# Kernel tuning notes

Hardware: AMD Instinct MI355X
Metric: run time of the kernel (lower is better)

Reference implementation:

```python
import jax, jax.numpy as jnp
import numpy as np

DIM = 256
HEADS = 4
WIN = 128
PAD = (WIN - 1) // 2  # 63
SHIFT = WIN // 2      # 64
RED = 16              # SE reduction


def _hann(w):
    # torch.hann_window(w, periodic=False)
    n = jnp.arange(w, dtype=jnp.float32)
    return 0.5 * (1.0 - jnp.cos(2.0 * jnp.pi * n / (w - 1)))


def _layernorm(x, g, b, eps=1e-5):
    mu = jnp.mean(x, axis=-1, keepdims=True)
    var = jnp.var(x, axis=-1, keepdims=True)
    return (x - mu) * jax.lax.rsqrt(var + eps) * g + b


def _attend_windows(x, ln_g, ln_b, in_proj_w, in_proj_b, out_w, out_b):
    B, T, C = x.shape
    w = WIN
    h = HEADS
    d = C // h
    L = T + 2 * PAD - w + 1  # number of stride-1 windows (= T-1 for even w)
    y = _layernorm(x, ln_g, ln_b)
    y_pad = jnp.pad(y, ((0, 0), (PAD, PAD), (0, 0)))
    idx = jnp.arange(L)[:, None] + jnp.arange(w)[None, :]  # (L, w)
    win = y_pad[:, idx, :]  # (B, L, w, C) -- the unfold blowup
    win = win * _hann(w)[None, None, :, None]
    # fused qkv projection (torch MHA in_proj)
    qkv = jnp.einsum('blwc,ec->blwe', win, in_proj_w) + in_proj_b  # (B,L,w,3C)
    q, k, v = jnp.split(qkv, 3, axis=-1)
    q = q.reshape(B, L, w, h, d)
    k = k.reshape(B, L, w, h, d)
    v = v.reshape(B, L, w, h, d)
    scale = 1.0 / jnp.sqrt(jnp.asarray(d, dtype=x.dtype))
    scores = jnp.einsum('blqhd,blkhd->blhqk', q, k) * scale
    attn = jax.nn.softmax(scores, axis=-1)
    o = jnp.einsum('blhqk,blkhd->blqhd', attn, v).reshape(B, L, w, C)
    o = jnp.einsum('blwc,ec->blwe', o, out_w) + out_b  # out_proj
    # fold: overlap-add back to length T (crop padding)
    idx_flat = idx.reshape(-1)  # (L*w,)
    acc = jnp.zeros((B, T + 2 * PAD, C), dtype=x.dtype)
    acc = acc.at[:, idx_flat, :].add(o.reshape(B, L * w, C))
    y_out = acc[:, PAD:PAD + T, :]
    counts = jnp.zeros((T + 2 * PAD,), dtype=x.dtype).at[idx_flat].add(1.0)
    counts = counts[PAD:PAD + T]
    return y_out / (counts[None, :, None] + 1e-6)


def setup_inputs() -> dict:
    key = jax.random.key(0)
    ks = jax.random.split(key, 9)
    C = DIM
    s = 0.02
    return {
        'x': jax.random.normal(ks[0], (1, 1024, C), dtype=jnp.float32),
        'ln_g': jnp.ones((C,), jnp.float32),
        'ln_b': jnp.zeros((C,), jnp.float32),
        'in_proj_w': jax.random.normal(ks[1], (3 * C, C), jnp.float32) * s,
        'in_proj_b': jnp.zeros((3 * C,), jnp.float32),
        'out_w': jax.random.normal(ks[2], (C, C), jnp.float32) * s,
        'out_b': jnp.zeros((C,), jnp.float32),
        'proj_w': jax.random.normal(ks[3], (C, C), jnp.float32) * s,
        'proj_b': jnp.zeros((C,), jnp.float32),
        'se_w1': jax.random.normal(ks[4], (C // RED, C), jnp.float32) * s,
        'se_w2': jax.random.normal(ks[5], (C, C // RED), jnp.float32) * s,
    }


def reference(x, ln_g, ln_b, in_proj_w, in_proj_b, out_w, out_b, proj_w, proj_b, se_w1, se_w2):
    # T > window_size branch (1024 > 128)
    y_main = _attend_windows(x, ln_g, ln_b, in_proj_w, in_proj_b, out_w, out_b)
    x_shift = jnp.roll(x, SHIFT, axis=1)
    y_shift = _attend_windows(x_shift, ln_g, ln_b, in_proj_w, in_proj_b, out_w, out_b)
    y_shift = jnp.roll(y_shift, -SHIFT, axis=1)
    y = 0.5 * (y_main + y_shift)
    y = jnp.einsum('btc,ec->bte', y, proj_w) + proj_b  # proj (dropout p=0 -> identity)
    # SE module: global average over T, bottleneck MLP, sigmoid gate
    s = jnp.mean(y, axis=1)  # (B, C)
    s = jax.nn.relu(s @ se_w1.T)
    s = jax.nn.sigmoid(s @ se_w2.T)
    y = y * s[:, None, :]
    return x + y
```

## Files before the change

### kernel.cpp

```cpp
#include <hip/hip_runtime.h>

#define TLEN 1024
#define CDIM 256
#define NHEAD 4
#define HD 64
#define WIN_ 128
#define PADL 63
#define LWIN 1023
#define TPAD 1150
#define SW 32

typedef __attribute__((ext_vector_type(8))) short bf16x8;
typedef __attribute__((ext_vector_type(4))) float f32x4;

__device__ __forceinline__ int prow(int v, int t) {
  if (v == 0) return t;
  if (t < PADL || t >= PADL + TLEN) return t;
  int s = t - PADL;
  s = (s + (TLEN - 64)) & (TLEN - 1);
  return PADL + s;
}

__device__ __forceinline__ float hannf(int j) {
  return 0.5f * (1.0f - __cosf(6.283185307179586f * (float)j / 127.0f));
}

__device__ __forceinline__ float countf(int t) {
  int lo = t - 127; if (lo < 0) lo = 0;
  int hi = t;       if (hi > LWIN - 1) hi = LWIN - 1;
  return (float)(hi - lo + 1);
}

__device__ __forceinline__ unsigned short bfr(float f) {
  unsigned int u = __float_as_uint(f);
  u += 0x7FFFu + ((u >> 16) & 1u);
  return (unsigned short)(u >> 16);
}
__device__ __forceinline__ unsigned int pk2t(float a, float b) {
  return __builtin_amdgcn_perm(__float_as_uint(b), __float_as_uint(a), 0x07060302u);
}
__device__ __forceinline__ float bfu(unsigned short u) {
  return __uint_as_float(((unsigned int)u) << 16);
}
__device__ __forceinline__ float bflo(unsigned int u) { return __uint_as_float(u << 16); }
__device__ __forceinline__ float bfhi(unsigned int u) { return __uint_as_float(u & 0xFFFF0000u); }

__device__ __forceinline__ float ex2(float x) {
  float r;
  asm("v_exp_f32 %0, %1" : "=v"(r) : "v"(x));
  return r;
}

#define AL16(h, l) ((((unsigned int)(l)) >> 16) | (((unsigned int)(h)) << 16))

#define QLOG2E 0.18033688011112042f

__global__ void k_prep(const float* __restrict__ x, const float* __restrict__ g,
                       const float* __restrict__ b, unsigned short* __restrict__ lnbf,
                       const float* __restrict__ W, unsigned short* __restrict__ Wb,
                       const float* __restrict__ pw, const float* __restrict__ ow,
                       const float* __restrict__ ob, unsigned short* __restrict__ Mtb,
                       float* __restrict__ vbv,
                       float* __restrict__ accg, unsigned short* __restrict__ Pbf,
                       float* __restrict__ msum) {
  __shared__ float pr[256];
  __shared__ float red[256];
  const int bid = blockIdx.x;
  const int tid = threadIdx.x;
  if (bid < 256) {
    int wv = tid >> 6, lane = tid & 63;
    int r = bid * 4 + wv;
    float4 v = ((const float4*)(x + (size_t)r * CDIM))[lane];
    float s = v.x + v.y + v.z + v.w;
    float q = v.x * v.x + v.y * v.y + v.z * v.z + v.w * v.w;
    #pragma unroll
    for (int m = 32; m >= 1; m >>= 1) { s += __shfl_xor(s, m); q += __shfl_xor(q, m); }
    float mu = s * (1.0f / 256.0f);
    float var = q * (1.0f / 256.0f) - mu * mu;
    float rs = rsqrtf(var + 1e-5f);
    float4 gg = ((const float4*)g)[lane];
    float4 bb = ((const float4*)b)[lane];
    uint2 o;
    o.x = (unsigned int)bfr((v.x - mu) * rs * gg.x + bb.x) |
          ((unsigned int)bfr((v.y - mu) * rs * gg.y + bb.y) << 16);
    o.y = (unsigned int)bfr((v.z - mu) * rs * gg.z + bb.z) |
          ((unsigned int)bfr((v.w - mu) * rs * gg.w + bb.w) << 16);
    ((uint2*)(lnbf + (size_t)r * CDIM))[lane] = o;
  } else if (bid < 352) {
    int i = (bid - 256) * 256 + tid;
    const float4* src = (const float4*)W;
    float4 a = src[2 * i], c = src[2 * i + 1];
    uint4 o;
    o.x = (unsigned int)bfr(a.x) | ((unsigned int)bfr(a.y) << 16);
    o.y = (unsigned int)bfr(a.z) | ((unsigned int)bfr(a.w) << 16);
    o.z = (unsigned int)bfr(c.x) | ((unsigned int)bfr(c.y) << 16);
    o.w = (unsigned int)bfr(c.z) | ((unsigned int)bfr(c.w) << 16);
    ((uint4*)Wb)[i] = o;
  } else if (bid < 608) {
    const int e = bid - 352;
    pr[tid] = pw[(size_t)e * CDIM + tid];
    __syncthreads();
    float a0 = 0.f, a1 = 0.f, a2 = 0.f, a3 = 0.f;
    for (int m = 0; m < 256; m += 4) {
      a0 += pr[m] * ow[(size_t)m * CDIM + tid];
      a1 += pr[m + 1] * ow[(size_t)(m + 1) * CDIM + tid];
      a2 += pr[m + 2] * ow[(size_t)(m + 2) * CDIM + tid];
      a3 += pr[m + 3] * ow[(size_t)(m + 3) * CDIM + tid];
    }
    Mtb[(size_t)e * CDIM + tid] = bfr((a0 + a1) + (a2 + a3));
    red[tid] = pr[tid] * ob[tid];
    __syncthreads();
    for (int s = 128; s > 0; s >>= 1) { if (tid < s) red[tid] += red[tid + s]; __syncthreads(); }
    if (tid == 0) vbv[e] = red[0];
  } else if (bid < 624) {
    uint4 zz = make_uint4(0, 0, 0, 0);
    for (int i = (bid - 608) * 256 + tid; i < 147200; i += 16 * 256)
      ((uint4*)accg)[i] = zz;
  } else {
    uint4 zz = make_uint4(0, 0, 0, 0);
    for (int i = (bid - 624) * 256 + tid; i < 12096; i += 16 * 256) {
      int idx = (i < 6048) ? i : (104352 + (i - 6048));
      ((uint4*)Pbf)[idx] = zz;
    }
    if (bid == 624 && tid < 64) ((float4*)msum)[tid] = make_float4(0.f, 0.f, 0.f, 0.f);
  }
}

__launch_bounds__(512, 1)
__global__ void k_proj(const unsigned short* __restrict__ lnbf,
                       const unsigned short* __restrict__ Wb,
                       unsigned short* __restrict__ Pbf) {
  __shared__ __align__(16) unsigned short Ps[64 * 128];
  const int tid = threadIdx.x;
  const int lane = tid & 63, wv = tid >> 6;
  const int li16 = lane & 15, q4 = lane >> 4;
  const int ws = wv & 1, we = wv >> 1;
  const int sbase = blockIdx.x * 64;
  const int ebase = blockIdx.y * 128;
  const int s0 = sbase + ws * 32;
  const int e0 = ebase + we * 32;

  f32x4 acc[2][2];
  #pragma unroll
  for (int it = 0; it < 2; ++it)
    #pragma unroll
    for (int et = 0; et < 2; ++et) acc[it][et] = (f32x4){0.f, 0.f, 0.f, 0.f};

  #pragma unroll
  for (int ks = 0; ks < 8; ++ks) {
    bf16x8 Af[2], Bf[2];
    #pragma unroll
    for (int it = 0; it < 2; ++it)
      Af[it] = *(const bf16x8*)(lnbf + (size_t)(s0 + 16 * it + li16) * 256 + ks * 32 + q4 * 8);
    #pragma unroll
    for (int et = 0; et < 2; ++et)
      Bf[et] = *(const bf16x8*)(Wb + (size_t)(e0 + 16 * et + li16) * 256 + ks * 32 + q4 * 8);
    #pragma unroll
    for (int it = 0; it < 2; ++it)
      #pragma unroll
      for (int et = 0; et < 2; ++et)
        acc[it][et] = __builtin_amdgcn_mfma_f32_16x16x32_bf16(Af[it], Bf[et], acc[it][et], 0, 0, 0);
  }
  #pragma unroll
  for (int it = 0; it < 2; ++it)
    #pragma unroll
    for (int et = 0; et < 2; ++et)
      #pragma unroll
      for (int r = 0; r < 4; ++r) {
        int lr = ws * 32 + 16 * it + 4 * q4 + r;
        int lc = we * 32 + 16 * et + li16;
        Ps[lr * 128 + lc] = bfr(acc[it][et][r]);
      }
  __syncthreads();
  for (int i = tid; i < 1024; i += 512) {
    int r = i >> 4, c = (i & 15) * 8;
    *(uint4*)(Pbf + (size_t)(PADL + sbase + r) * 768 + ebase + c) = *(uint4*)&Ps[r * 128 + c];
  }
}

__device__ __forceinline__ void stage_load(const unsigned short* __restrict__ Pbf,
                                           int v, int hd, int l0, int w, int tid,
                                           uint4& A, uint4& B) {
  const int jp = tid & 63;
  const int dg = tid >> 6;
  const int j0 = 2 * jp;
  int row0 = prow(v, l0 + w + j0);
  int row1 = prow(v, l0 + w + j0 + 1);
  A = *(const uint4*)(Pbf + (size_t)row0 * 768 + 512 + hd * 64 + dg * 8);
  B = *(const uint4*)(Pbf + (size_t)row1 * 768 + 512 + hd * 64 + dg * 8);
}

__device__ __forceinline__ void stage_write(unsigned short* vt, int w, int tid,
                                            const float* __restrict__ bB,
                                            const float* __restrict__ hth,
                                            uint4 a, uint4 b) {
  const int jp = tid & 63;
  const int dg = tid >> 6;
  const int j0 = 2 * jp;
  const int p0 = w + j0;
  float h0 = hth[j0], h1 = hth[j0 + 1];
  float e0 = ex2(h0 * bB[p0]);
  float e1 = ex2(h1 * bB[p0 + 1]);
  float f0 = e0 * h0, f1 = e1 * h1;
  unsigned int av[4] = {a.x, a.y, a.z, a.w};
  unsigned int bv[4] = {b.x, b.y, b.z, b.w};
  #pragma unroll
  for (int q = 0; q < 4; ++q) {
    int d0 = dg * 8 + 2 * q;
    unsigned int w0 = pk2t(f0 * bflo(av[q]), f1 * bflo(bv[q]));
    unsigned int w1 = pk2t(f0 * bfhi(av[q]), f1 * bfhi(bv[q]));
    *(unsigned int*)&vt[d0 * 128 + (j0 ^ ((d0 & 7) << 3))] = w0;
    *(unsigned int*)&vt[(d0 + 1) * 128 + (j0 ^ (((d0 + 1) & 7) << 3))] = w1;
  }
  if (tid < 64) {
    *(unsigned int*)&vt[64 * 128 + j0] = pk2t(e0, e1);
  }
}

__launch_bounds__(512, 2)
__global__ void k_attn(const unsigned short* __restrict__ Pbf, const float* __restrict__ ipb,
                       float* __restrict__ accg) {
  __shared__ __align__(16) unsigned short band[160 * 168];
  __shared__ __align__(16) unsigned short Vt[2][80 * 128];
  __shared__ __align__(16) unsigned char uni[159 * 68 * 4];
  __shared__ float hth[128];
  __shared__ float bB[160];
  __shared__ float bqS[64];

  unsigned short* Pq = (unsigned short*)uni;
  unsigned short* Pk = Pq + 159 * 64;
  float* accs = (float*)uni;

  const int strip = blockIdx.x, hd = blockIdx.y, v = blockIdx.z;
  const int l0 = strip * SW;
  const int nw = (SW < LWIN - l0) ? SW : (LWIN - l0);
  const int span = nw - 1 + WIN_;
  const int tid = threadIdx.x;
  const int lane = tid & 63, wv = tid >> 6;
  const int li16 = lane & 15, q4 = lane >> 4;
  const int iw = 16 * wv + li16;

  uint4 sA, sB;
  stage_load(Pbf, v, hd, l0, 0, tid, sA, sB);

  if (tid < 128) hth[tid] = hannf(tid);
  if (tid < 64) bqS[tid] = ipb[hd * 64 + tid];
  for (int i = tid; i < span * 8; i += 512) {
    int t = i >> 3, dg = i & 7;
    int row = prow(v, l0 + t);
    const unsigned short* src = Pbf + (size_t)row * 768 + hd * 64;
    uint4 q = *(const uint4*)(src + dg * 8);
    uint4 k = *(const uint4*)(src + 256 + dg * 8);
    int off = (dg * 8) ^ ((t & 7) << 3);
    *(uint4*)&Pq[t * 64 + off] = q;
    *(uint4*)&Pk[t * 64 + off] = k;
  }
  {
    uint4 zz = make_uint4(0, 0, 0, 0);
    for (int i = tid; i < 480; i += 512) {
      int bidx = i / 240, k = i % 240;
      *(uint4*)&Vt[bidx][65 * 128 + k * 8] = zz;
    }
  }
  __syncthreads();

  for (int p = tid; p < span; p += 512) {
    float b = 0.0f;
    int sw = (p & 7) << 3;
    for (int d = 0; d < 64; ++d) b += bqS[d] * bfu(Pk[p * 64 + (d ^ sw)]);
    bB[p] = b * QLOG2E;
  }
  for (int tile = wv; tile < 100; tile += 8) {
    int ta = tile / 10, tb = tile - 10 * (tile / 10);
    int tqa = 16 * ta + li16, swq = (tqa & 7) << 3;
    bf16x8 Aq0 = *(bf16x8*)&Pq[tqa * 64 + ((8 * q4) ^ swq)];
    bf16x8 Aq1 = *(bf16x8*)&Pq[tqa * 64 + ((32 + 8 * q4) ^ swq)];
    int tkb = 16 * tb + li16, swk = (tkb & 7) << 3;
    bf16x8 Bk0 = *(bf16x8*)&Pk[tkb * 64 + ((8 * q4) ^ swk)];
    bf16x8 Bk1 = *(bf16x8*)&Pk[tkb * 64 + ((32 + 8 * q4) ^ swk)];
    f32x4 D = (f32x4){0.f, 0.f, 0.f, 0.f};
    D = __builtin_amdgcn_mfma_f32_16x16x32_bf16(Aq0, Bk0, D, 0, 0, 0);
    D = __builtin_amdgcn_mfma_f32_16x16x32_bf16(Aq1, Bk1, D, 0, 0, 0);
    #pragma unroll
    for (int r = 0; r < 4; ++r)
      band[(16 * ta + 4 * q4 + r) * 168 + 16 * tb + li16] = bfr(D[r]);
  }
  __syncthreads();

  for (int i = tid; i < 159 * 68; i += 512) accs[i] = 0.0f;
  stage_write(&Vt[0][0], 0, tid, bB, hth, sA, sB);
  __syncthreads();

  float hh2[32];
  {
    const float h_i = hth[iw];
    #pragma unroll
    for (int ks = 0; ks < 4; ++ks)
      #pragma unroll
      for (int jj = 0; jj < 8; ++jj)
        hh2[ks * 8 + jj] = h_i * hth[32 * ks + 8 * q4 + jj] * QLOG2E;
  }

  #pragma unroll 1
  for (int w = 0; w < nw; ++w) {
    if (w + 1 < nw) stage_load(Pbf, v, hd, l0, w + 1, tid, sA, sB);

    const int m = w & 7;
    const unsigned short* brow = &band[(w + iw) * 168 + (w & ~7)];
    const unsigned short* vt = &Vt[w & 1][0];

    f32x4 O[5];
    #pragma unroll
    for (int mt = 0; mt < 5; ++mt) O[mt] = (f32x4){0.f, 0.f, 0.f, 0.f};

    #pragma unroll
    for (int ks = 0; ks < 4; ++ks) {
      uint4 R0 = *(const uint4*)&brow[32 * ks + 8 * q4];
      uint4 R1 = *(const uint4*)&brow[32 * ks + 8 * q4 + 8];
      unsigned int d0 = R0.x, d1 = R0.y, d2 = R0.z, d3 = R0.w;
      unsigned int d4 = R1.x, d5 = R1.y, d6 = R1.z, d7 = R1.w;
      unsigned int o0, o1, o2, o3;
      switch (m) {
        case 0: o0 = d0; o1 = d1; o2 = d2; o3 = d3; break;
        case 1: o0 = AL16(d1, d0); o1 = AL16(d2, d1); o2 = AL16(d3, d2); o3 = AL16(d4, d3); break;
        case 2: o0 = d1; o1 = d2; o2 = d3; o3 = d4; break;
        case 3: o0 = AL16(d2, d1); o1 = AL16(d3, d2); o2 = AL16(d4, d3); o3 = AL16(d5, d4); break;
        case 4: o0 = d2; o1 = d3; o2 = d4; o3 = d5; break;
        case 5: o0 = AL16(d3, d2); o1 = AL16(d4, d3); o2 = AL16(d5, d4); o3 = AL16(d6, d5); break;
        case 6: o0 = d3; o1 = d4; o2 = d5; o3 = d6; break;
        default: o0 = AL16(d4, d3); o1 = AL16(d5, d4); o2 = AL16(d6, d5); o3 = AL16(d7, d6); break;
      }
      float a0 = ex2(hh2[ks * 8 + 0] * bflo(o0));
      float a1 = ex2(hh2[ks * 8 + 1] * bfhi(o0));
      float a2 = ex2(hh2[ks * 8 + 2] * bflo(o1));
      float a3 = ex2(hh2[ks * 8 + 3] * bfhi(o1));
      float a4 = ex2(hh2[ks * 8 + 4] * bflo(o2));
      float a5 = ex2(hh2[ks * 8 + 5] * bfhi(o2));
      float a6 = ex2(hh2[ks * 8 + 6] * bflo(o3));
      float a7 = ex2(hh2[ks * 8 + 7] * bfhi(o3));
      union { uint4 u; bf16x8 f; } cvt;
      cvt.u.x = pk2t(a0, a1);
      cvt.u.y = pk2t(a2, a3);
      cvt.u.z = pk2t(a4, a5);
      cvt.u.w = pk2t(a6, a7);
      bf16x8 Bf = cvt.f;

      #pragma unroll
      for (int mt = 0; mt < 5; ++mt) {
        int d = 16 * mt + li16;
        bf16x8 Af = *(bf16x8*)&vt[d * 128 + ((32 * ks + 8 * q4) ^ ((d & 7) << 3))];
        O[mt] = __builtin_amdgcn_mfma_f32_16x16x32_bf16(Af, Bf, O[mt], 0, 0, 0);
      }
    }

    float nn = __shfl(O[4][0], li16);
    float sc = 1.0f / nn;

    {
      float* arow = &accs[(w + iw) * 68];
      #pragma unroll
      for (int mt = 0; mt < 4; ++mt) {
        int c = 16 * mt + 4 * q4;
        float4 cur = *(float4*)&arow[c];
        cur.x += O[mt][0] * sc; cur.y += O[mt][1] * sc;
        cur.z += O[mt][2] * sc; cur.w += O[mt][3] * sc;
        *(float4*)&arow[c] = cur;
      }
    }

    if (w + 1 < nw) stage_write(&Vt[(w + 1) & 1][0], w + 1, tid, bB, hth, sA, sB);
    __syncthreads();
  }

  float* av = accg + (size_t)v * TPAD * CDIM;
  for (int i = tid; i < span * 64; i += 512) {
    int p = i >> 6, dd = i & 63;
    int lo = p - 127; if (lo < 0) lo = 0;
    int hi = p; if (hi > nw - 1) hi = nw - 1;
    float cnt = (float)(hi - lo + 1);
    float bvd = ipb[512 + hd * 64 + dd];
    atomicAdd(&av[(size_t)(l0 + p) * CDIM + hd * 64 + dd],
              accs[p * 68 + dd] + cnt * bvd);
  }
}

__launch_bounds__(512, 2)
__global__ void k_comb(const float* __restrict__ accg, const unsigned short* __restrict__ Mtb,
                       const float* __restrict__ vbv, const float* __restrict__ pb,
                       float* __restrict__ z, float* __restrict__ msum) {
  __shared__ __align__(16) unsigned short Ub[32 * 264];
  __shared__ float cfA[32], cfB[32], bscL[32];
  __shared__ float msB[128];
  const int tid = threadIdx.x;
  const int lane = tid & 63, wv = tid >> 6;
  const int li16 = lane & 15, q4 = lane >> 4;
  const int t0 = blockIdx.x * 32;
  const int e0 = blockIdx.y * 128;

  if (tid < 32) {
    int s = t0 + tid;
    float c0 = countf(PADL + s);
    float c1 = countf(PADL + ((s + 64) & (TLEN - 1)));
    float fA = 0.5f / (c0 + 1e-6f), fB = 0.5f / (c1 + 1e-6f);
    cfA[tid] = fA; cfB[tid] = fB;
    bscL[tid] = c0 * fA + c1 * fB;
  }
  if (tid < 128) msB[tid] = 0.0f;
  __syncthreads();

  for (int i = tid; i < 32 * 128; i += 512) {
    int rr = i >> 7, c2 = (i & 127) * 2;
    int s = t0 + rr;
    int s1 = (s + 64) & (TLEN - 1);
    float2 a0 = *(const float2*)&accg[(size_t)(PADL + s) * CDIM + c2];
    float2 a1 = *(const float2*)&accg[(size_t)TPAD * CDIM + (size_t)(PADL + s1) * CDIM + c2];
    float fA = cfA[rr], fB = cfB[rr];
    *(unsigned int*)&Ub[rr * 264 + c2] =
        pk2t(a0.x * fA + a1.x * fB, a0.y * fA + a1.y * fB);
  }
  __syncthreads();

  f32x4 acc[2];
  acc[0] = (f32x4){0.f, 0.f, 0.f, 0.f};
  acc[1] = (f32x4){0.f, 0.f, 0.f, 0.f};
  #pragma unroll
  for (int ks = 0; ks < 8; ++ks) {
    bf16x8 Bf = *(const bf16x8*)(Mtb + (size_t)(e0 + wv * 16 + li16) * 256 + ks * 32 + q4 * 8);
    #pragma unroll
    for (int it = 0; it < 2; ++it) {
      bf16x8 Af = *(bf16x8*)&Ub[(16 * it + li16) * 264 + ks * 32 + q4 * 8];
      acc[it] = __builtin_amdgcn_mfma_f32_16x16x32_bf16(Af, Bf, acc[it], 0, 0, 0);
    }
  }

  {
    int e = e0 + wv * 16 + li16;
    float vbe = vbv[e], pbe = pb[e];
    float part = 0.0f;
    #pragma unroll
    for (int it = 0; it < 2; ++it)
      #pragma unroll
      for (int r = 0; r < 4; ++r) {
        int rloc = 16 * it + 4 * q4 + r;
        float val = acc[it][r] + bscL[rloc] * vbe + pbe;
        z[(size_t)(t0 + rloc) * CDIM + e] = val;
        part += val;
      }
    atomicAdd(&msB[e - e0], part);
  }
  __syncthreads();
  if (tid < 128) atomicAdd(&msum[e0 + tid], msB[tid]);
}

__global__ void k_finalse(const float* __restrict__ x, const float* __restrict__ z,
                          const float* __restrict__ msum, const float* __restrict__ w1,
                          const float* __restrict__ w2, float* __restrict__ out) {
  __shared__ float red2[16][4];
  __shared__ float s1[16];
  __shared__ float gateS[256];
  int tid = threadIdx.x;
  int lane = tid & 63, wv = tid >> 6;
  float sm = msum[tid] * (1.0f / 1024.0f);
  #pragma unroll
  for (int r = 0; r < 16; ++r) {
    float v = sm * w1[(size_t)r * 256 + tid];
    #pragma unroll
    for (int m = 32; m >= 1; m >>= 1) v += __shfl_xor(v, m);
    if (lane == 0) red2[r][wv] = v;
  }
  __syncthreads();
  if (tid < 16) {
    float a = red2[tid][0] + red2[tid][1] + red2[tid][2] + red2[tid][3];
    s1[tid] = fmaxf(a, 0.0f);
  }
  __syncthreads();
  float gacc = 0.0f;
  #pragma unroll
  for (int i = 0; i < 16; ++i) gacc += s1[i] * w2[(size_t)tid * 16 + i];
  gateS[tid] = 1.0f / (1.0f + __expf(-gacc));
  __syncthreads();
  int i = blockIdx.x * 256 + tid;
  float4 xv = ((const float4*)x)[i];
  float4 zv = ((const float4*)z)[i];
  float4 gv = ((const float4*)gateS)[i & 63];
  float4 o;
  o.x = xv.x + zv.x * gv.x;
  o.y = xv.y + zv.y * gv.y;
  o.z = xv.z + zv.z * gv.z;
  o.w = xv.w + zv.w * gv.w;
  ((float4*)out)[i] = o;
}

extern "C" void kernel_launch(void* const* d_in, const int* in_sizes, int n_in,
                              void* d_out, int out_size, void* d_ws, size_t ws_size,
                              hipStream_t stream) {
  const float* x   = (const float*)d_in[0];
  const float* lng = (const float*)d_in[1];
  const float* lnb = (const float*)d_in[2];
  const float* ipw = (const float*)d_in[3];
  const float* ipb = (const float*)d_in[4];
  const float* ow  = (const float*)d_in[5];
  const float* ob  = (const float*)d_in[6];
  const float* pw  = (const float*)d_in[7];
  const float* pb  = (const float*)d_in[8];
  const float* w1  = (const float*)d_in[9];
  const float* w2  = (const float*)d_in[10];
  float* out = (float*)d_out;

  float* ws = (float*)d_ws;
  unsigned short* lnbf = (unsigned short*)ws;
  unsigned short* Wb   = (unsigned short*)(ws + 131072);
  unsigned short* Pbf  = (unsigned short*)(ws + 229376);
  float* accg = ws + 229376 + 441600;
  unsigned short* Mtb = (unsigned short*)(accg + 588800);
  float* vbv  = accg + 588800 + 32768;
  float* z    = vbv + 256;
  float* msum = z + 262144;

  k_prep<<<dim3(640), dim3(256), 0, stream>>>(x, lng, lnb, lnbf, ipw, Wb,
                                              pw, ow, ob, Mtb, vbv, accg, Pbf, msum);
  k_proj<<<dim3(16, 6), dim3(512), 0, stream>>>(lnbf, Wb, Pbf);
  k_attn<<<dim3(32, NHEAD, 2), dim3(512), 0, stream>>>(Pbf, ipb, accg);
  k_comb<<<dim3(32, 2), dim3(512), 0, stream>>>(accg, Mtb, vbv, pb, z, msum);
  k_finalse<<<dim3(256), dim3(256), 0, stream>>>(x, z, msum, w1, w2, out);
}
```

Baseline: 179.5 us.

## Compute softmax denominator with VALU dot instead of an extra MFMA tile

The softmax normaliser was computed as a fifth MFMA row-tile (an exp-weight row padded with zeros in Vt). It is now a per-lane fp32 dot product of the attention weights with an fp32 E32 buffer, reduced across lanes with shuffles and inverted with v_rcp_f32. This drops one MFMA per k-step and shrinks Vt shared memory. It also prefetches the accumulator row before the MFMAs and splits the bias dot-product across thread pairs. The change trades MFMA work for extra VALU FMAs and LDS reads, and it changes denominator precision from a bf16 operand to fp32.

```diff
diff --git a/kernel.cpp b/kernel.cpp
--- a/kernel.cpp
+++ b/kernel.cpp
@@ -48,6 +48,11 @@
 __device__ __forceinline__ float ex2(float x) {
   float r;
   asm("v_exp_f32 %0, %1" : "=v"(r) : "v"(x));
+  return r;
+}
+__device__ __forceinline__ float rcpf(float x) {
+  float r;
+  asm("v_rcp_f32 %0, %1" : "=v"(r) : "v"(x));
   return r;
 }
 
@@ -190,7 +195,7 @@
   B = *(const uint4*)(Pbf + (size_t)row1 * 768 + 512 + hd * 64 + dg * 8);
 }
 
-__device__ __forceinline__ void stage_write(unsigned short* vt, int w, int tid,
+__device__ __forceinline__ void stage_write(unsigned short* vt, float* ev, int w, int tid,
                                             const float* __restrict__ bB,
                                             const float* __restrict__ hth,
                                             uint4 a, uint4 b) {
@@ -213,7 +218,7 @@
     *(unsigned int*)&vt[(d0 + 1) * 128 + (j0 ^ (((d0 + 1) & 7) << 3))] = w1;
   }
   if (tid < 64) {
-    *(unsigned int*)&vt[64 * 128 + j0] = pk2t(e0, e1);
+    *(float2*)&ev[j0] = make_float2(e0, e1);
   }
 }
 
@@ -221,8 +226,9 @@
 __global__ void k_attn(const unsigned short* __restrict__ Pbf, const float* __restrict__ ipb,
                        float* __restrict__ accg) {
   __shared__ __align__(16) unsigned short band[160 * 168];
-  __shared__ __align__(16) unsigned short Vt[2][80 * 128];
+  __shared__ __align__(16) unsigned short Vt[2][64 * 128];
   __shared__ __align__(16) unsigned char uni[159 * 68 * 4];
+  __shared__ __align__(16) float E32[2][128];
   __shared__ float hth[128];
   __shared__ float bB[160];
   __shared__ float bqS[64];
@@ -255,20 +261,18 @@
     *(uint4*)&Pq[t * 64 + off] = q;
     *(uint4*)&Pk[t * 64 + off] = k;
   }
+  __syncthreads();
+
   {
-    uint4 zz = make_uint4(0, 0, 0, 0);
-    for (int i = tid; i < 480; i += 512) {
-      int bidx = i / 240, k = i % 240;
-      *(uint4*)&Vt[bidx][65 * 128 + k * 8] = zz;
+    int p = tid >> 1, h = tid & 1;
+    float s = 0.0f;
+    if (p < span) {
+      int sw = (p & 7) << 3;
+      int d0 = 32 * h;
+      for (int d = d0; d < d0 + 32; ++d) s += bqS[d] * bfu(Pk[p * 64 + (d ^ sw)]);
     }
-  }
-  __syncthreads();
-
-  for (int p = tid; p < span; p += 512) {
-    float b = 0.0f;
-    int sw = (p & 7) << 3;
-    for (int d = 0; d < 64; ++d) b += bqS[d] * bfu(Pk[p * 64 + (d ^ sw)]);
-    bB[p] = b * QLOG2E;
+    s += __shfl_xor(s, 1);
+    if (p < span && h == 0) bB[p] = s * QLOG2E;
   }
   for (int tile = wv; tile < 100; tile += 8) {
     int ta = tile / 10, tb = tile - 10 * (tile / 10);
@@ -288,7 +292,7 @@
   __syncthreads();
 
   for (int i = tid; i < 159 * 68; i += 512) accs[i] = 0.0f;
-  stage_write(&Vt[0][0], 0, tid, bB, hth, sA, sB);
+  stage_write(&Vt[0][0], E32[0], 0, tid, bB, hth, sA, sB);
   __syncthreads();
 
   float hh2[32];
@@ -308,10 +312,18 @@
     const int m = w & 7;
     const unsigned short* brow = &band[(w + iw) * 168 + (w & ~7)];
     const unsigned short* vt = &Vt[w & 1][0];
-
-    f32x4 O[5];
-    #pragma unroll
-    for (int mt = 0; mt < 5; ++mt) O[mt] = (f32x4){0.f, 0.f, 0.f, 0.f};
+    const float* Ev = E32[w & 1];
+    float* arow = &accs[(w + iw) * 68];
+
+    float4 cur[4];
+    #pragma unroll
+    for (int mt = 0; mt < 4; ++mt) cur[mt] = *(float4*)&arow[16 * mt + 4 * q4];
+
+    f32x4 O[4];
+    #pragma unroll
+    for (int mt = 0; mt < 4; ++mt) O[mt] = (f32x4){0.f, 0.f, 0.f, 0.f};
+
+    float nnp = 0.0f;
 
     #pragma unroll
     for (int ks = 0; ks < 4; ++ks) {
@@ -338,6 +350,12 @@
       float a5 = ex2(hh2[ks * 8 + 5] * bfhi(o2));
       float a6 = ex2(hh2[ks * 8 + 6] * bflo(o3));
       float a7 = ex2(hh2[ks * 8 + 7] * bfhi(o3));
+      {
+        float4 E0 = *(const float4*)&Ev[32 * ks + 8 * q4];
+        float4 E1 = *(const float4*)&Ev[32 * ks + 8 * q4 + 4];
+        nnp += a0 * E0.x + a1 * E0.y + a2 * E0.z + a3 * E0.w
+             + a4 * E1.x + a5 * E1.y + a6 * E1.z + a7 * E1.w;
+      }
       union { uint4 u; bf16x8 f; } cvt;
       cvt.u.x = pk2t(a0, a1);
       cvt.u.y = pk2t(a2, a3);
@@ -346,29 +364,29 @@
       bf16x8 Bf = cvt.f;
 
       #pragma unroll
-      for (int mt = 0; mt < 5; ++mt) {
+      for (int mt = 0; mt < 4; ++mt) {
         int d = 16 * mt + li16;
         bf16x8 Af = *(bf16x8*)&vt[d * 128 + ((32 * ks + 8 * q4) ^ ((d & 7) << 3))];
         O[mt] = __builtin_amdgcn_mfma_f32_16x16x32_bf16(Af, Bf, O[mt], 0, 0, 0);
       }
     }
 
-    float nn = __shfl(O[4][0], li16);
-    float sc = 1.0f / nn;
-
-    {
-      float* arow = &accs[(w + iw) * 68];
-      #pragma unroll
-      for (int mt = 0; mt < 4; ++mt) {
-        int c = 16 * mt + 4 * q4;
-        float4 cur = *(float4*)&arow[c];
-        cur.x += O[mt][0] * sc; cur.y += O[mt][1] * sc;
-        cur.z += O[mt][2] * sc; cur.w += O[mt][3] * sc;
-        *(float4*)&arow[c] = cur;
-      }
+    float t = nnp;
+    t += __shfl_xor(t, 16);
+    t += __shfl_xor(t, 32);
+    float sc = rcpf(t);
+
+    #pragma unroll
+    for (int mt = 0; mt < 4; ++mt) {
+      int c = 16 * mt + 4 * q4;
+      float4 u = cur[mt];
+      u.x += O[mt][0] * sc; u.y += O[mt][1] * sc;
+      u.z += O[mt][2] * sc; u.w += O[mt][3] * sc;
+      *(float4*)&arow[c] = u;
     }
 
-    if (w + 1 < nw) stage_write(&Vt[(w + 1) & 1][0], w + 1, tid, bB, hth, sA, sB);
+    if (w + 1 < nw)
+      stage_write(&Vt[(w + 1) & 1][0], E32[(w + 1) & 1], w + 1, tid, bB, hth, sA, sB);
     __syncthreads();
   }
 
```

Measured after the change: 183.9 us. +2.4%, slower.

## Process two windows per loop iteration to halve barriers and interleave MFMAs

Applied to the files above, without the earlier changes.

The per-window attention loop now handles a pair of windows per iteration. Both V tiles are staged ahead of time, and the two windows' exp/MFMA chains are interleaved so the work can overlap and the per-window barrier cost is amortised. The accumulator read for the first window is hoisted before the compute, and an extra barrier separates the two overlapping accumulator row updates. The cost is higher register pressure from two sets of accumulators and staged loads, which may reduce occupancy under the 512-thread launch bounds.

```diff
diff --git a/kernel.cpp b/kernel.cpp
--- a/kernel.cpp
+++ b/kernel.cpp
@@ -240,8 +240,9 @@
   const int li16 = lane & 15, q4 = lane >> 4;
   const int iw = 16 * wv + li16;
 
-  uint4 sA, sB;
-  stage_load(Pbf, v, hd, l0, 0, tid, sA, sB);
+  uint4 sA0, sB0, sA1, sB1;
+  stage_load(Pbf, v, hd, l0, 0, tid, sA0, sB0);
+  stage_load(Pbf, v, hd, l0, 1, tid, sA1, sB1);
 
   if (tid < 128) hth[tid] = hannf(tid);
   if (tid < 64) bqS[tid] = ipb[hd * 64 + tid];
@@ -288,7 +289,8 @@
   __syncthreads();
 
   for (int i = tid; i < 159 * 68; i += 512) accs[i] = 0.0f;
-  stage_write(&Vt[0][0], 0, tid, bB, hth, sA, sB);
+  stage_write(&Vt[0][0], 0, tid, bB, hth, sA0, sB0);
+  stage_write(&Vt[1][0], 1, tid, bB, hth, sA1, sB1);
   __syncthreads();
 
   float hh2[32];
@@ -301,74 +303,122 @@
         hh2[ks * 8 + jj] = h_i * hth[32 * ks + 8 * q4 + jj] * QLOG2E;
   }
 
+  const unsigned short* vt0 = &Vt[0][0];
+  const unsigned short* vt1 = &Vt[1][0];
+
   #pragma unroll 1
-  for (int w = 0; w < nw; ++w) {
-    if (w + 1 < nw) stage_load(Pbf, v, hd, l0, w + 1, tid, sA, sB);
-
-    const int m = w & 7;
-    const unsigned short* brow = &band[(w + iw) * 168 + (w & ~7)];
-    const unsigned short* vt = &Vt[w & 1][0];
-
-    f32x4 O[5];
-    #pragma unroll
-    for (int mt = 0; mt < 5; ++mt) O[mt] = (f32x4){0.f, 0.f, 0.f, 0.f};
+  for (int wp = 0; wp < nw; wp += 2) {
+    const bool has1 = (wp + 1 < nw);
+    if (wp + 2 < nw) stage_load(Pbf, v, hd, l0, wp + 2, tid, sA0, sB0);
+    if (wp + 3 < nw) stage_load(Pbf, v, hd, l0, wp + 3, tid, sA1, sB1);
+
+    const int s = (wp & 7) >> 1;
+    const unsigned short* br0 = &band[(wp + iw) * 168 + (wp & ~7)];
+    const unsigned short* br1 = br0 + 168;
+
+    float* arow0 = &accs[(wp + iw) * 68];
+    float4 cur0[4];
+    #pragma unroll
+    for (int mt = 0; mt < 4; ++mt) cur0[mt] = *(float4*)&arow0[16 * mt + 4 * q4];
+
+    f32x4 O0[5], O1[5];
+    #pragma unroll
+    for (int mt = 0; mt < 5; ++mt) {
+      O0[mt] = (f32x4){0.f, 0.f, 0.f, 0.f};
+      O1[mt] = (f32x4){0.f, 0.f, 0.f, 0.f};
+    }
 
     #pragma unroll
     for (int ks = 0; ks < 4; ++ks) {
-      uint4 R0 = *(const uint4*)&brow[32 * ks + 8 * q4];
-      uint4 R1 = *(const uint4*)&brow[32 * ks + 8 * q4 + 8];
-      unsigned int d0 = R0.x, d1 = R0.y, d2 = R0.z, d3 = R0.w;
-      unsigned int d4 = R1.x, d5 = R1.y, d6 = R1.z, d7 = R1.w;
-      unsigned int o0, o1, o2, o3;
-      switch (m) {
-        case 0: o0 = d0; o1 = d1; o2 = d2; o3 = d3; break;
-        case 1: o0 = AL16(d1, d0); o1 = AL16(d2, d1); o2 = AL16(d3, d2); o3 = AL16(d4, d3); break;
-        case 2: o0 = d1; o1 = d2; o2 = d3; o3 = d4; break;
-        case 3: o0 = AL16(d2, d1); o1 = AL16(d3, d2); o2 = AL16(d4, d3); o3 = AL16(d5, d4); break;
-        case 4: o0 = d2; o1 = d3; o2 = d4; o3 = d5; break;
-        case 5: o0 = AL16(d3, d2); o1 = AL16(d4, d3); o2 = AL16(d5, d4); o3 = AL16(d6, d5); break;
-        case 6: o0 = d3; o1 = d4; o2 = d5; o3 = d6; break;
-        default: o0 = AL16(d4, d3); o1 = AL16(d5, d4); o2 = AL16(d6, d5); o3 = AL16(d7, d6); break;
+      uint4 P0 = *(const uint4*)&br0[32 * ks + 8 * q4];
+      uint4 P1 = *(const uint4*)&br0[32 * ks + 8 * q4 + 8];
+      uint4 Q0 = *(const uint4*)&br1[32 * ks + 8 * q4];
+      uint4 Q1 = *(const uint4*)&br1[32 * ks + 8 * q4 + 8];
+      unsigned int p0 = P0.x, p1 = P0.y, p2 = P0.z, p3 = P0.w, p4 = P1.x, p5 = P1.y, p6 = P1.z;
+      unsigned int q0 = Q0.x, q1 = Q0.y, q2 = Q0.z, q3 = Q0.w, q4r = Q1.x, q5 = Q1.y, q6 = Q1.z;
+      unsigned int e0, e1, e2, e3;
+      unsigned int f0, f1, f2, f3;
+      switch (s) {
+        case 0:
+          e0 = p0; e1 = p1; e2 = p2; e3 = p3;
+          f0 = AL16(q1, q0); f1 = AL16(q2, q1); f2 = AL16(q3, q2); f3 = AL16(q4r, q3);
+          break;
+        case 1:
+          e0 = p1; e1 = p2; e2 = p3; e3 = p4;
+          f0 = AL16(q2, q1); f1 = AL16(q3, q2); f2 = AL16(q4r, q3); f3 = AL16(q5, q4r);
+          break;
+        case 2:
+          e0 = p2; e1 = p3; e2 = p4; e3 = p5;
+          f0 = AL16(q3, q2); f1 = AL16(q4r, q3); f2 = AL16(q5, q4r); f3 = AL16(q6, q5);
+          break;
+        default:
+          e0 = p3; e1 = p4; e2 = p5; e3 = p6;
+          f0 = AL16(q4r, q3); f1 = AL16(q5, q4r); f2 = AL16(q6, q5); f3 = AL16(Q1.w, q6);
+          break;
       }
-      float a0 = ex2(hh2[ks * 8 + 0] * bflo(o0));
-      float a1 = ex2(hh2[ks * 8 + 1] * bfhi(o0));
-      float a2 = ex2(hh2[ks * 8 + 2] * bflo(o1));
-      float a3 = ex2(hh2[ks * 8 + 3] * bfhi(o1));
-      float a4 = ex2(hh2[ks * 8 + 4] * bflo(o2));
-      float a5 = ex2(hh2[ks * 8 + 5] * bfhi(o2));
-      float a6 = ex2(hh2[ks * 8 + 6] * bflo(o3));
-      float a7 = ex2(hh2[ks * 8 + 7] * bfhi(o3));
-      union { uint4 u; bf16x8 f; } cvt;
-      cvt.u.x = pk2t(a0, a1);
-      cvt.u.y = pk2t(a2, a3);
-      cvt.u.z = pk2t(a4, a5);
-      cvt.u.w = pk2t(a6, a7);
-      bf16x8 Bf = cvt.f;
+      float a0 = ex2(hh2[ks * 8 + 0] * bflo(e0));
+      float a1 = ex2(hh2[ks * 8 + 1] * bfhi(e0));
+      float a2 = ex2(hh2[ks * 8 + 2] * bflo(e1));
+      float a3 = ex2(hh2[ks * 8 + 3] * bfhi(e1));
+      float a4 = ex2(hh2[ks * 8 + 4] * bflo(e2));
+      float a5 = ex2(hh2[ks * 8 + 5] * bfhi(e2));
+      float a6 = ex2(hh2[ks * 8 + 6] * bflo(e3));
+      float a7 = ex2(hh2[ks * 8 + 7] * bfhi(e3));
+      float b0 = ex2(hh2[ks * 8 + 0] * bflo(f0));
+      float b1 = ex2(hh2[ks * 8 + 1] * bfhi(f0));
+      float b2 = ex2(hh2[ks * 8 + 2] * bflo(f1));
+      float b3 = ex2(hh2[ks * 8 + 3] * bfhi(f1));
+      float b4 = ex2(hh2[ks * 8 + 4] * bflo(f2));
+      float b5 = ex2(hh2[ks * 8 + 5] * bfhi(f2));
+      float b6 = ex2(hh2[ks * 8 + 6] * bflo(f3));
+      float b7 = ex2(hh2[ks * 8 + 7] * bfhi(f3));
+      union { uint4 u; bf16x8 fr; } c0, c1;
+      c0.u.x = pk2t(a0, a1); c0.u.y = pk2t(a2, a3);
+      c0.u.z = pk2t(a4, a5); c0.u.w = pk2t(a6, a7);
+      c1.u.x = pk2t(b0, b1); c1.u.y = pk2t(b2, b3);
+      c1.u.z = pk2t(b4, b5); c1.u.w = pk2t(b6, b7);
+      bf16x8 Bf0 = c0.fr, Bf1 = c1.fr;
 
       #pragma unroll
       for (int mt = 0; mt < 5; ++mt) {
         int d = 16 * mt + li16;
-        bf16x8 Af = *(bf16x8*)&vt[d * 128 + ((32 * ks + 8 * q4) ^ ((d & 7) << 3))];
-        O[mt] = __builtin_amdgcn_mfma_f32_16x16x32_bf16(Af, Bf, O[mt], 0, 0, 0);
+        int off = (32 * ks + 8 * q4) ^ ((d & 7) << 3);
+        bf16x8 Af0 = *(const bf16x8*)&vt0[d * 128 + off];
+        O0[mt] = __builtin_amdgcn_mfma_f32_16x16x32_bf16(Af0, Bf0, O0[mt], 0, 0, 0);
+        bf16x8 Af1 = *(const bf16x8*)&vt1[d * 128 + off];
+        O1[mt] = __builtin_amdgcn_mfma_f32_16x16x32_bf16(Af1, Bf1, O1[mt], 0, 0, 0);
       }
     }
 
-    float nn = __shfl(O[4][0], li16);
-    float sc = 1.0f / nn;
-
     {
-      float* arow = &accs[(w + iw) * 68];
+      float nn = __shfl(O0[4][0], li16);
+      float sc = 1.0f / nn;
       #pragma unroll
       for (int mt = 0; mt < 4; ++mt) {
         int c = 16 * mt + 4 * q4;
-        float4 cur = *(float4*)&arow[c];
-        cur.x += O[mt][0] * sc; cur.y += O[mt][1] * sc;
-        cur.z += O[mt][2] * sc; cur.w += O[mt][3] * sc;
-        *(float4*)&arow[c] = cur;
+        float4 u = cur0[mt];
+        u.x += O0[mt][0] * sc; u.y += O0[mt][1] * sc;
+        u.z += O0[mt][2] * sc; u.w += O0[mt][3] * sc;
+        *(float4*)&arow0[c] = u;
       }
     }
-
-    if (w + 1 < nw) stage_write(&Vt[(w + 1) & 1][0], w + 1, tid, bB, hth, sA, sB);
+    __syncthreads();
+
+    if (has1) {
+      float nn = __shfl(O1[4][0], li16);
+      float sc = 1.0f / nn;
+      float* arow1 = &accs[(wp + 1 + iw) * 68];
+      #pragma unroll
+      for (int mt = 0; mt < 4; ++mt) {
+        int c = 16 * mt + 4 * q4;
+        float4 u = *(float4*)&arow1[c];
+        u.x += O1[mt][0] * sc; u.y += O1[mt][1] * sc;
+        u.z += O1[mt][2] * sc; u.w += O1[mt][3] * sc;
+        *(float4*)&arow1[c] = u;
+      }
+    }
+    if (wp + 2 < nw) stage_write(&Vt[0][0], wp + 2, tid, bB, hth, sA0, sB0);
+    if (wp + 3 < nw) stage_write(&Vt[1][0], wp + 3, tid, bB, hth, sA1, sB1);
     __syncthreads();
   }
 
```

New measurement: 186.3 us. 3.8% more time.

## Process two attention windows concurrently with two 512-thread wave groups

Applied to the files above, without the earlier changes.

k_attn now launches 1024 threads, split into two wave groups that each handle one window per iteration (w = wp + wg). Each group stages its own V tile into its own buffer. The two groups serialize their accumulation into shared memory across an extra barrier. This is meant to halve the sequential window loop and raise wave-level parallelism per block. In exchange, per-window double buffering of the next V load is gone, the loop needs two barriers per step, and launch_bounds(1024,4) tightens the register budget, so hh2 and the accumulators may spill.

```diff
diff --git a/kernel.cpp b/kernel.cpp
--- a/kernel.cpp
+++ b/kernel.cpp
@@ -179,10 +179,10 @@
 }
 
 __device__ __forceinline__ void stage_load(const unsigned short* __restrict__ Pbf,
-                                           int v, int hd, int l0, int w, int tid,
+                                           int v, int hd, int l0, int w, int stid,
                                            uint4& A, uint4& B) {
-  const int jp = tid & 63;
-  const int dg = tid >> 6;
+  const int jp = stid & 63;
+  const int dg = stid >> 6;
   const int j0 = 2 * jp;
   int row0 = prow(v, l0 + w + j0);
   int row1 = prow(v, l0 + w + j0 + 1);
@@ -190,12 +190,12 @@
   B = *(const uint4*)(Pbf + (size_t)row1 * 768 + 512 + hd * 64 + dg * 8);
 }
 
-__device__ __forceinline__ void stage_write(unsigned short* vt, int w, int tid,
+__device__ __forceinline__ void stage_write(unsigned short* vt, int w, int stid,
                                             const float* __restrict__ bB,
                                             const float* __restrict__ hth,
                                             uint4 a, uint4 b) {
-  const int jp = tid & 63;
-  const int dg = tid >> 6;
+  const int jp = stid & 63;
+  const int dg = stid >> 6;
   const int j0 = 2 * jp;
   const int p0 = w + j0;
   float h0 = hth[j0], h1 = hth[j0 + 1];
@@ -212,12 +212,12 @@
     *(unsigned int*)&vt[d0 * 128 + (j0 ^ ((d0 & 7) << 3))] = w0;
     *(unsigned int*)&vt[(d0 + 1) * 128 + (j0 ^ (((d0 + 1) & 7) << 3))] = w1;
   }
-  if (tid < 64) {
+  if (stid < 64) {
     *(unsigned int*)&vt[64 * 128 + j0] = pk2t(e0, e1);
   }
 }
 
-__launch_bounds__(512, 2)
+__launch_bounds__(1024, 4)
 __global__ void k_attn(const unsigned short* __restrict__ Pbf, const float* __restrict__ ipb,
                        float* __restrict__ accg) {
   __shared__ __align__(16) unsigned short band[160 * 168];
@@ -236,16 +236,20 @@
   const int nw = (SW < LWIN - l0) ? SW : (LWIN - l0);
   const int span = nw - 1 + WIN_;
   const int tid = threadIdx.x;
-  const int lane = tid & 63, wv = tid >> 6;
+  const int lane = tid & 63;
+  const int wv16 = tid >> 6;
+  const int wg = wv16 >> 3;
+  const int wv = wv16 & 7;
+  const int stid = tid & 511;
   const int li16 = lane & 15, q4 = lane >> 4;
   const int iw = 16 * wv + li16;
 
   uint4 sA, sB;
-  stage_load(Pbf, v, hd, l0, 0, tid, sA, sB);
+  stage_load(Pbf, v, hd, l0, wg, stid, sA, sB);
 
   if (tid < 128) hth[tid] = hannf(tid);
   if (tid < 64) bqS[tid] = ipb[hd * 64 + tid];
-  for (int i = tid; i < span * 8; i += 512) {
+  for (int i = tid; i < span * 8; i += 1024) {
     int t = i >> 3, dg = i & 7;
     int row = prow(v, l0 + t);
     const unsigned short* src = Pbf + (size_t)row * 768 + hd * 64;
@@ -257,20 +261,20 @@
   }
   {
     uint4 zz = make_uint4(0, 0, 0, 0);
-    for (int i = tid; i < 480; i += 512) {
+    for (int i = tid; i < 480; i += 1024) {
       int bidx = i / 240, k = i % 240;
       *(uint4*)&Vt[bidx][65 * 128 + k * 8] = zz;
     }
   }
   __syncthreads();
 
-  for (int p = tid; p < span; p += 512) {
+  for (int p = tid; p < span; p += 1024) {
     float b = 0.0f;
     int sw = (p & 7) << 3;
     for (int d = 0; d < 64; ++d) b += bqS[d] * bfu(Pk[p * 64 + (d ^ sw)]);
     bB[p] = b * QLOG2E;
   }
-  for (int tile = wv; tile < 100; tile += 8) {
+  for (int tile = wv16; tile < 100; tile += 16) {
     int ta = tile / 10, tb = tile - 10 * (tile / 10);
     int tqa = 16 * ta + li16, swq = (tqa & 7) << 3;
     bf16x8 Aq0 = *(bf16x8*)&Pq[tqa * 64 + ((8 * q4) ^ swq)];
@@ -287,8 +291,9 @@
   }
   __syncthreads();
 
-  for (int i = tid; i < 159 * 68; i += 512) accs[i] = 0.0f;
-  stage_write(&Vt[0][0], 0, tid, bB, hth, sA, sB);
+  for (int i = tid; i < 159 * 68; i += 1024) accs[i] = 0.0f;
+  if (wg == 0) stage_write(&Vt[0][0], 0, stid, bB, hth, sA, sB);
+  else         stage_write(&Vt[1][0], 1, stid, bB, hth, sA, sB);
   __syncthreads();
 
   float hh2[32];
@@ -302,61 +307,65 @@
   }
 
   #pragma unroll 1
-  for (int w = 0; w < nw; ++w) {
-    if (w + 1 < nw) stage_load(Pbf, v, hd, l0, w + 1, tid, sA, sB);
-
-    const int m = w & 7;
-    const unsigned short* brow = &band[(w + iw) * 168 + (w & ~7)];
-    const unsigned short* vt = &Vt[w & 1][0];
+  for (int wp = 0; wp < nw; wp += 2) {
+    const int w = wp + wg;
+    const bool act = (w < nw);
+    const int wnext = wp + 2 + wg;
+    if (wnext < nw) stage_load(Pbf, v, hd, l0, wnext, stid, sA, sB);
 
     f32x4 O[5];
     #pragma unroll
     for (int mt = 0; mt < 5; ++mt) O[mt] = (f32x4){0.f, 0.f, 0.f, 0.f};
 
-    #pragma unroll
-    for (int ks = 0; ks < 4; ++ks) {
-      uint4 R0 = *(const uint4*)&brow[32 * ks + 8 * q4];
-      uint4 R1 = *(const uint4*)&brow[32 * ks + 8 * q4 + 8];
-      unsigned int d0 = R0.x, d1 = R0.y, d2 = R0.z, d3 = R0.w;
-      unsigned int d4 = R1.x, d5 = R1.y, d6 = R1.z, d7 = R1.w;
-      unsigned int o0, o1, o2, o3;
-      switch (m) {
-        case 0: o0 = d0; o1 = d1; o2 = d2; o3 = d3; break;
-        case 1: o0 = AL16(d1, d0); o1 = AL16(d2, d1); o2 = AL16(d3, d2); o3 = AL16(d4, d3); break;
-        case 2: o0 = d1; o1 = d2; o2 = d3; o3 = d4; break;
-        case 3: o0 = AL16(d2, d1); o1 = AL16(d3, d2); o2 = AL16(d4, d3); o3 = AL16(d5, d4); break;
-        case 4: o0 = d2; o1 = d3; o2 = d4; o3 = d5; break;
-        case 5: o0 = AL16(d3, d2); o1 = AL16(d4, d3); o2 = AL16(d5, d4); o3 = AL16(d6, d5); break;
-        case 6: o0 = d3; o1 = d4; o2 = d5; o3 = d6; break;
-        default: o0 = AL16(d4, d3); o1 = AL16(d5, d4); o2 = AL16(d6, d5); o3 = AL16(d7, d6); break;
+    if (act) {
+      const int m = w & 7;
+      const unsigned short* brow = &band[(w + iw) * 168 + (w & ~7)];
+      const unsigned short* vt = &Vt[wg][0];
+
+      #pragma unroll
+      for (int ks = 0; ks < 4; ++ks) {
+        uint4 R0 = *(const uint4*)&brow[32 * ks + 8 * q4];
+        uint4 R1 = *(const uint4*)&brow[32 * ks + 8 * q4 + 8];
+        unsigned int d0 = R0.x, d1 = R0.y, d2 = R0.z, d3 = R0.w;
+        unsigned int d4 = R1.x, d5 = R1.y, d6 = R1.z, d7 = R1.w;
+        unsigned int o0, o1, o2, o3;
+        switch (m) {
+          case 0: o0 = d0; o1 = d1; o2 = d2; o3 = d3; break;
+          case 1: o0 = AL16(d1, d0); o1 = AL16(d2, d1); o2 = AL16(d3, d2); o3 = AL16(d4, d3); break;
+          case 2: o0 = d1; o1 = d2; o2 = d3; o3 = d4; break;
+          case 3: o0 = AL16(d2, d1); o1 = AL16(d3, d2); o2 = AL16(d4, d3); o3 = AL16(d5, d4); break;
+          case 4: o0 = d2; o1 = d3; o2 = d4; o3 = d5; break;
+          case 5: o0 = AL16(d3, d2); o1 = AL16(d4, d3); o2 = AL16(d5, d4); o3 = AL16(d6, d5); break;
+          case 6: o0 = d3; o1 = d4; o2 = d5; o3 = d6; break;
+          default: o0 = AL16(d4, d3); o1 = AL16(d5, d4); o2 = AL16(d6, d5); o3 = AL16(d7, d6); break;
+        }
+        float a0 = ex2(hh2[ks * 8 + 0] * bflo(o0));
+        float a1 = ex2(hh2[ks * 8 + 1] * bfhi(o0));
+        float a2 = ex2(hh2[ks * 8 + 2] * bflo(o1));
+        float a3 = ex2(hh2[ks * 8 + 3] * bfhi(o1));
+        float a4 = ex2(hh2[ks * 8 + 4] * bflo(o2));
+        float a5 = ex2(hh2[ks * 8 + 5] * bfhi(o2));
+        float a6 = ex2(hh2[ks * 8 + 6] * bflo(o3));
+        float a7 = ex2(hh2[ks * 8 + 7] * bfhi(o3));
+        union { uint4 u; bf16x8 f; } cvt;
+        cvt.u.x = pk2t(a0, a1);
+        cvt.u.y = pk2t(a2, a3);
+        cvt.u.z = pk2t(a4, a5);
+        cvt.u.w = pk2t(a6, a7);
+        bf16x8 Bf = cvt.f;
+
+        #pragma unroll
+        for (int mt = 0; mt < 5; ++mt) {
+          int d = 16 * mt + li16;
+          bf16x8 Af = *(bf16x8*)&vt[d * 128 + ((32 * ks + 8 * q4) ^ ((d & 7) << 3))];
+          O[mt] = __builtin_amdgcn_mfma_f32_16x16x32_bf16(Af, Bf, O[mt], 0, 0, 0);
+        }
       }
-      float a0 = ex2(hh2[ks * 8 + 0] * bflo(o0));
-      float a1 = ex2(hh2[ks * 8 + 1] * bfhi(o0));
-      float a2 = ex2(hh2[ks * 8 + 2] * bflo(o1));
-      float a3 = ex2(hh2[ks * 8 + 3] * bfhi(o1));
-      float a4 = ex2(hh2[ks * 8 + 4] * bflo(o2));
-      float a5 = ex2(hh2[ks * 8 + 5] * bfhi(o2));
-      float a6 = ex2(hh2[ks * 8 + 6] * bflo(o3));
-      float a7 = ex2(hh2[ks * 8 + 7] * bfhi(o3));
-      union { uint4 u; bf16x8 f; } cvt;
-      cvt.u.x = pk2t(a0, a1);
-      cvt.u.y = pk2t(a2, a3);
-      cvt.u.z = pk2t(a4, a5);
-      cvt.u.w = pk2t(a6, a7);
-      bf16x8 Bf = cvt.f;
-
-      #pragma unroll
-      for (int mt = 0; mt < 5; ++mt) {
-        int d = 16 * mt + li16;
-        bf16x8 Af = *(bf16x8*)&vt[d * 128 + ((32 * ks + 8 * q4) ^ ((d & 7) << 3))];
-        O[mt] = __builtin_amdgcn_mfma_f32_16x16x32_bf16(Af, Bf, O[mt], 0, 0, 0);
-      }
-    }
-
-    float nn = __shfl(O[4][0], li16);
-    float sc = 1.0f / nn;
-
-    {
+    }
+
+    if (wg == 0) {
+      float nn = __shfl(O[4][0], li16);
+      float sc = 1.0f / nn;
       float* arow = &accs[(w + iw) * 68];
       #pragma unroll
       for (int mt = 0; mt < 4; ++mt) {
@@ -367,13 +376,27 @@
         *(float4*)&arow[c] = cur;
       }
     }
-
-    if (w + 1 < nw) stage_write(&Vt[(w + 1) & 1][0], w + 1, tid, bB, hth, sA, sB);
     __syncthreads();
+
+    if (wg == 1 && act) {
+      float nn = __shfl(O[4][0], li16);
+      float sc = 1.0f / nn;
+      float* arow = &accs[(w + iw) * 68];
+      #pragma unroll
+      for (int mt = 0; mt < 4; ++mt) {
+        int c = 16 * mt + 4 * q4;
+        float4 cur = *(float4*)&arow[c];
+        cur.x += O[mt][0] * sc; cur.y += O[mt][1] * sc;
+        cur.z += O[mt][2] * sc; cur.w += O[mt][3] * sc;
+        *(float4*)&arow[c] = cur;
+      }
+    }
+    if (wnext < nw) stage_write(&Vt[wg][0], wnext, stid, bB, hth, sA, sB);
+    __syncthreads();
   }
 
   float* av = accg + (size_t)v * TPAD * CDIM;
-  for (int i = tid; i < span * 64; i += 512) {
+  for (int i = tid; i < span * 64; i += 1024) {
     int p = i >> 6, dd = i & 63;
     int lo = p - 127; if (lo < 0) lo = 0;
     int hi = p; if (hi > nw - 1) hi = nw - 1;
@@ -520,7 +543,7 @@
   k_prep<<<dim3(640), dim3(256), 0, stream>>>(x, lng, lnb, lnbf, ipw, Wb,
                                               pw, ow, ob, Mtb, vbv, accg, Pbf, msum);
   k_proj<<<dim3(16, 6), dim3(512), 0, stream>>>(lnbf, Wb, Pbf);
-  k_attn<<<dim3(32, NHEAD, 2), dim3(512), 0, stream>>>(Pbf, ipb, accg);
+  k_attn<<<dim3(32, NHEAD, 2), dim3(1024), 0, stream>>>(Pbf, ipb, accg);
   k_comb<<<dim3(32, 2), dim3(512), 0, stream>>>(accg, Mtb, vbv, pb, z, msum);
   k_finalse<<<dim3(256), dim3(256), 0, stream>>>(x, z, msum, w1, w2, out);
 }
```

New measurement: 173.8 us. 1.03x faster.
